# Kernel optimization log

Hardware: AMD Instinct MI355X
Metric: run time of the kernel (lower is better)

## Reference

```python
import jax, jax.numpy as jnp
import numpy as np

N_NODES = 100000
N_EDGES = 3200000
IN_DIM = 11
HID = 32


def setup_inputs() -> dict:
    key = jax.random.key(0)
    ks = jax.random.split(key, 12)
    inp = {
        "x": jax.random.normal(ks[0], (N_NODES, IN_DIM), dtype=jnp.float32),
        "edge_index": jax.random.randint(ks[1], (2, N_EDGES), 0, N_NODES, dtype=jnp.int32),
        "batch": jnp.zeros((N_NODES,), dtype=jnp.int32),
        # GCNConv layer 1 (11 -> 32)
        "W1": jax.random.normal(ks[2], (IN_DIM, HID), dtype=jnp.float32) / np.sqrt(IN_DIM),
        "b1": jnp.zeros((HID,), dtype=jnp.float32),
        # GCNConv layer 2 (32 -> 32)
        "W2": jax.random.normal(ks[3], (HID, HID), dtype=jnp.float32) / np.sqrt(HID),
        "b2": jnp.zeros((HID,), dtype=jnp.float32),
        # output MLP: 32 -> 16 -> 1
        "Wo1": jax.random.normal(ks[4], (HID, HID // 2), dtype=jnp.float32) / np.sqrt(HID),
        "bo1": jnp.zeros((HID // 2,), dtype=jnp.float32),
        "Wo2": jax.random.normal(ks[5], (HID // 2, 1), dtype=jnp.float32) / np.sqrt(HID // 2),
        "bo2": jnp.zeros((1,), dtype=jnp.float32),
    }
    return inp


def _gcn_norm(edge_index, n_nodes):
    # Add self-loops and compute symmetric normalization (PyG GCNConv default).
    loops = jnp.arange(n_nodes, dtype=edge_index.dtype)
    src = jnp.concatenate([edge_index[0], loops])
    dst = jnp.concatenate([edge_index[1], loops])
    ones = jnp.ones_like(dst, dtype=jnp.float32)
    deg = jax.ops.segment_sum(ones, dst, num_segments=n_nodes)  # degree of A+I on target side
    dinv = jax.lax.rsqrt(deg)  # deg >= 1 thanks to self-loops
    norm = dinv[src] * dinv[dst]  # [E+N]
    return src, dst, norm


def _gcn_conv(x, W, b, src, dst, norm, n_nodes):
    xw = x @ W                                   # transform first (small dim)
    msg = norm[:, None] * xw[src]                # gather + scale  [E+N, H]
    agg = jax.ops.segment_sum(msg, dst, num_segments=n_nodes)  # scatter-add
    return agg + b


def reference(x, edge_index, batch, W1, b1, W2, b2, Wo1, bo1, Wo2, bo2):
    n = x.shape[0]
    src, dst, norm = _gcn_norm(edge_index, n)
    h = jax.nn.relu(_gcn_conv(x, W1, b1, src, dst, norm, n))
    # F.dropout(training=self.training) is identity in eval mode
    h = jax.nn.relu(_gcn_conv(h, W2, b2, src, dst, norm, n))
    h = jax.nn.elu(h @ Wo1 + bo1)
    out = h @ Wo2 + bo2
    return out.squeeze(-1)  # [N]
```

## Files before the change

### kernel.cpp

```cpp
#include <hip/hip_runtime.h>
#include <hip/hip_fp16.h>
#include <math.h>

#define N_NODES 100000
#define N_EDGES 3200000
#define IN_DIM 11
#define HID 32
#define HID2 16
#define SCHUNK 100352
#define BINSHIFT 8
#define BINSZ 256
#define NB 391
#define CHUNK 8192

__global__ __launch_bounds__(1024) void k_hist(const int* __restrict__ ei,
                                               int* __restrict__ bincnt) {
    __shared__ int h[NB];
    for (int i = threadIdx.x; i < NB; i += 1024) h[i] = 0;
    __syncthreads();
    int b0 = blockIdx.x * CHUNK;
    int e1 = b0 + CHUNK; if (e1 > N_EDGES) e1 = N_EDGES;
    for (int e = b0 + threadIdx.x; e < e1; e += 1024)
        atomicAdd(&h[ei[N_EDGES + e] >> BINSHIFT], 1);
    __syncthreads();
    for (int i = threadIdx.x; i < NB; i += 1024)
        if (h[i]) atomicAdd(&bincnt[i], h[i]);
}

__global__ __launch_bounds__(1024) void k_binscatter(const int* __restrict__ ei,
                                                     const int* __restrict__ bincnt,
                                                     int* __restrict__ bincur,
                                                     unsigned* __restrict__ binbuf) {
    __shared__ int pre[NB];
    __shared__ int h[NB];
    __shared__ int base[NB];
    __shared__ int tmp[512];
    int tid = threadIdx.x;
    int v = (tid < NB) ? bincnt[tid] : 0;
    if (tid < 512) tmp[tid] = v;
    __syncthreads();
    for (int off = 1; off < 512; off <<= 1) {
        int t = (tid < 512 && tid >= off) ? tmp[tid - off] : 0;
        __syncthreads();
        if (tid < 512) tmp[tid] += t;
        __syncthreads();
    }
    if (tid < NB) pre[tid] = tmp[tid] - v;
    for (int i = tid; i < NB; i += 1024) h[i] = 0;
    __syncthreads();
    int b0 = blockIdx.x * CHUNK;
    int e1 = b0 + CHUNK; if (e1 > N_EDGES) e1 = N_EDGES;
    for (int e = b0 + tid; e < e1; e += 1024)
        atomicAdd(&h[ei[N_EDGES + e] >> BINSHIFT], 1);
    __syncthreads();
    for (int i = tid; i < NB; i += 1024) {
        int c = h[i];
        if (c) base[i] = pre[i] + atomicAdd(&bincur[i], c);
        h[i] = 0;
    }
    __syncthreads();
    for (int e = b0 + tid; e < e1; e += 1024) {
        int d = ei[N_EDGES + e];
        int s = ei[e];
        int b = d >> BINSHIFT;
        int p = base[b] + atomicAdd(&h[b], 1);
        binbuf[p] = (unsigned)s | ((unsigned)(d & (BINSZ - 1)) << 17);
    }
}

__global__ __launch_bounds__(1024) void k_binfill(const unsigned* __restrict__ binbuf,
                                                  const int* __restrict__ bincnt,
                                                  int* __restrict__ rowstart,
                                                  float* __restrict__ dinv,
                                                  int* __restrict__ csr_src) {
    int b = blockIdx.x;
    int tid = threadIdx.x;
    __shared__ int tmp[512];
    __shared__ int cnt[BINSZ];
    __shared__ int rloc[BINSZ];
    __shared__ int cur[BINSZ];
    int v = (tid < 512 && tid < b) ? bincnt[tid] : 0;
    if (tid < 512) tmp[tid] = v;
    __syncthreads();
    for (int off = 256; off >= 1; off >>= 1) {
        if (tid < off) tmp[tid] += tmp[tid + off];
        __syncthreads();
    }
    int ebeg = tmp[0];
    int eend = ebeg + bincnt[b];
    __syncthreads();
    if (tid < BINSZ) cnt[tid] = 0;
    __syncthreads();
    for (int e = ebeg + tid; e < eend; e += 1024)
        atomicAdd(&cnt[binbuf[e] >> 17], 1);
    __syncthreads();
    int c = (tid < BINSZ) ? cnt[tid] : 0;
    if (tid < BINSZ) tmp[tid] = c;
    __syncthreads();
    for (int off = 1; off < BINSZ; off <<= 1) {
        int t = (tid < BINSZ && tid >= off) ? tmp[tid - off] : 0;
        __syncthreads();
        if (tid < BINSZ) tmp[tid] += t;
        __syncthreads();
    }
    if (tid < BINSZ) {
        rloc[tid] = tmp[tid] - c;
        cur[tid] = 0;
        int node = b * BINSZ + tid;
        if (node < N_NODES) {
            rowstart[node] = ebeg + rloc[tid];
            dinv[node] = rsqrtf((float)c + 1.0f);
        }
    }
    if (b == 0 && tid == 0) rowstart[N_NODES] = N_EDGES;
    __syncthreads();
    for (int e = ebeg + tid; e < eend; e += 1024) {
        unsigned vv = binbuf[e];
        int dl = vv >> 17;
        int s = (int)(vv & 0x1FFFFu);
        int p = ebeg + rloc[dl] + atomicAdd(&cur[dl], 1);
        csr_src[p] = s;
    }
}

__global__ void k_xw1(const float* __restrict__ x, const float* __restrict__ W1,
                      const float* __restrict__ dinv, __half* __restrict__ xwh) {
    int t = blockIdx.x * blockDim.x + threadIdx.x;
    int node = t >> 5;
    int j = t & 31;
    __shared__ float sW[IN_DIM * HID];
    __shared__ float sx[8 * IN_DIM];
    for (int i = threadIdx.x; i < IN_DIM * HID; i += 256) sW[i] = W1[i];
    int base = blockIdx.x * 8;
    if (threadIdx.x < 8 * IN_DIM) sx[threadIdx.x] = x[base * IN_DIM + threadIdx.x];
    __syncthreads();
    int ln = node - base;
    float acc = 0.0f;
#pragma unroll
    for (int k = 0; k < IN_DIM; ++k)
        acc += sx[ln * IN_DIM + k] * sW[k * HID + j];
    xwh[t] = __float2half(dinv[node] * acc);
}

__device__ __forceinline__ void accum8(float* __restrict__ acc, const uint4 v) {
    float2 f0 = __half22float2(*(const __half2*)&v.x);
    float2 f1 = __half22float2(*(const __half2*)&v.y);
    float2 f2 = __half22float2(*(const __half2*)&v.z);
    float2 f3 = __half22float2(*(const __half2*)&v.w);
    acc[0] += f0.x; acc[1] += f0.y;
    acc[2] += f1.x; acc[3] += f1.y;
    acc[4] += f2.x; acc[5] += f2.y;
    acc[6] += f3.x; acc[7] += f3.y;
}

__device__ __forceinline__ void edge_accum8(int beg, int end, int q, int oj,
                                            const int* __restrict__ csr_src,
                                            const __half* __restrict__ xwh,
                                            float* __restrict__ acc) {
#pragma unroll
    for (int k = 0; k < 8; ++k) acc[k] = 0.0f;
    int e = beg;
    for (; e + 32 <= end; e += 32) {
        int s0 = csr_src[e + q];
        int s1 = csr_src[e + 8 + q];
        int s2 = csr_src[e + 16 + q];
        int s3 = csr_src[e + 24 + q];
        uint4 v0 = *(const uint4*)(xwh + ((s0 << 5) | oj));
        uint4 v1 = *(const uint4*)(xwh + ((s1 << 5) | oj));
        uint4 v2 = *(const uint4*)(xwh + ((s2 << 5) | oj));
        uint4 v3 = *(const uint4*)(xwh + ((s3 << 5) | oj));
        accum8(acc, v0); accum8(acc, v1); accum8(acc, v2); accum8(acc, v3);
    }
    if (e + 16 <= end) {
        int s0 = csr_src[e + q];
        int s1 = csr_src[e + 8 + q];
        uint4 v0 = *(const uint4*)(xwh + ((s0 << 5) | oj));
        uint4 v1 = *(const uint4*)(xwh + ((s1 << 5) | oj));
        accum8(acc, v0); accum8(acc, v1);
        e += 16;
    }
    if (e + 8 <= end) {
        int s0 = csr_src[e + q];
        uint4 v0 = *(const uint4*)(xwh + ((s0 << 5) | oj));
        accum8(acc, v0);
        e += 8;
    }
    if (e + q < end) {
        int s0 = csr_src[e + q];
        uint4 v0 = *(const uint4*)(xwh + ((s0 << 5) | oj));
        accum8(acc, v0);
    }
#pragma unroll
    for (int m = 4; m <= 16; m <<= 1) {
#pragma unroll
        for (int k = 0; k < 8; ++k) acc[k] += __shfl_xor(acc[k], m);
    }
}

__global__ __launch_bounds__(256) void k_gather_xw2(const int* __restrict__ rowstart,
                                                    const float* __restrict__ dinv,
                                                    const int* __restrict__ csr_src,
                                                    const __half* __restrict__ xwh1,
                                                    const float* __restrict__ b1,
                                                    const float* __restrict__ W2,
                                                    __half* __restrict__ xwh2) {
    __shared__ float sW2[HID * HID];
    __shared__ float sA[8][33];
    __shared__ float sH[8][33];
    for (int i = threadIdx.x; i < HID * HID; i += 256) sW2[i] = W2[i];

    int ln = threadIdx.x >> 5;
    int node = blockIdx.x * 8 + ln;
    int l = threadIdx.x & 31;
    int q = l >> 2;
    int oj = (l & 3) << 3;

    float acc[8];
    edge_accum8(rowstart[node], rowstart[node + 1], q, oj, csr_src, xwh1, acc);
    if (q == 0) {
#pragma unroll
        for (int k = 0; k < 8; ++k) sA[ln][oj + k] = acc[k];
    }
    __syncthreads();

    int j = l;
    float dd = dinv[node];
    float hv = dd * (sA[ln][j] + __half2float(xwh1[node * HID + j])) + b1[j];
    sH[ln][j] = hv > 0.0f ? hv : 0.0f;
    __syncthreads();

    float a2 = 0.0f;
#pragma unroll
    for (int k = 0; k < HID; ++k) a2 += sH[ln][k] * sW2[k * HID + j];
    xwh2[node * HID + j] = __float2half(dd * a2);
}

__global__ __launch_bounds__(256) void k_gather_mlp(const int* __restrict__ rowstart,
                                                    const float* __restrict__ dinv,
                                                    const int* __restrict__ csr_src,
                                                    const __half* __restrict__ xwh,
                                                    const float* __restrict__ b2,
                                                    const float* __restrict__ Wo1,
                                                    const float* __restrict__ bo1,
                                                    const float* __restrict__ Wo2,
                                                    const float* __restrict__ bo2,
                                                    float* __restrict__ out) {
    __shared__ float sW1[HID * HID2];
    __shared__ float sb1[HID2];
    __shared__ float sW2v[HID2];
    __shared__ float sb2[HID];
    __shared__ float sA[8][33];
    __shared__ float sH[8][33];
    for (int i = threadIdx.x; i < HID * HID2; i += 256) sW1[i] = Wo1[i];
    if (threadIdx.x < HID2) {
        sb1[threadIdx.x] = bo1[threadIdx.x];
        sW2v[threadIdx.x] = Wo2[threadIdx.x];
    }
    if (threadIdx.x < HID) sb2[threadIdx.x] = b2[threadIdx.x];

    int ln = threadIdx.x >> 5;
    int node = blockIdx.x * 8 + ln;
    int l = threadIdx.x & 31;
    int q = l >> 2;
    int oj = (l & 3) << 3;

    float acc[8];
    edge_accum8(rowstart[node], rowstart[node + 1], q, oj, csr_src, xwh, acc);
    if (q == 0) {
#pragma unroll
        for (int k = 0; k < 8; ++k) sA[ln][oj + k] = acc[k];
    }
    __syncthreads();

    int j = l;
    float dd = dinv[node];
    float hv = dd * (sA[ln][j] + __half2float(xwh[node * HID + j])) + sb2[j];
    sH[ln][j] = hv > 0.0f ? hv : 0.0f;
    __syncthreads();

    float val = 0.0f;
    if (j < HID2) {
        float a = sb1[j];
#pragma unroll
        for (int k = 0; k < HID; ++k) a += sH[ln][k] * sW1[k * HID2 + j];
        a = a > 0.0f ? a : (expf(a) - 1.0f);
        val = a * sW2v[j];
    }
#pragma unroll
    for (int d = 16; d >= 1; d >>= 1) val += __shfl_down(val, d, 32);
    if (j == 0) out[node] = val + bo2[0];
}

extern "C" void kernel_launch(void* const* d_in, const int* in_sizes, int n_in,
                              void* d_out, int out_size, void* d_ws, size_t ws_size,
                              hipStream_t stream) {
    const float* x   = (const float*)d_in[0];
    const int*   ei  = (const int*)d_in[1];
    const float* W1  = (const float*)d_in[3];
    const float* b1  = (const float*)d_in[4];
    const float* W2  = (const float*)d_in[5];
    const float* b2  = (const float*)d_in[6];
    const float* Wo1 = (const float*)d_in[7];
    const float* bo1 = (const float*)d_in[8];
    const float* Wo2 = (const float*)d_in[9];
    const float* bo2 = (const float*)d_in[10];
    float* out = (float*)d_out;

    int*      bincnt   = (int*)d_ws;
    int*      bincur   = bincnt + 512;
    int*      rowstart = bincur + 512;
    float*    dinv     = (float*)(rowstart + SCHUNK);
    int*      csr_src  = (int*)(dinv + SCHUNK);
    unsigned* binbuf   = (unsigned*)(csr_src + N_EDGES);
    __half*   XWH1     = (__half*)(binbuf + N_EDGES);
    __half*   XWH2     = XWH1 + (size_t)N_NODES * HID;

    const int BT = 256;
    int gNH  = (N_NODES * HID + BT - 1) / BT;
    int gC   = (N_EDGES + CHUNK - 1) / CHUNK;
    int gG   = N_NODES / 8;

    hipMemsetAsync(bincnt, 0, 1024 * sizeof(int), stream);
    k_hist      <<<gC, 1024, 0, stream>>>(ei, bincnt);
    k_binscatter<<<gC, 1024, 0, stream>>>(ei, bincnt, bincur, binbuf);
    k_binfill   <<<NB, 1024, 0, stream>>>(binbuf, bincnt, rowstart, dinv, csr_src);

    k_xw1<<<gNH, BT, 0, stream>>>(x, W1, dinv, XWH1);
    k_gather_xw2<<<gG, BT, 0, stream>>>(rowstart, dinv, csr_src, XWH1, b1, W2, XWH2);

    k_gather_mlp<<<gG, BT, 0, stream>>>(rowstart, dinv, csr_src, XWH2,
                                        b2, Wo1, bo1, Wo2, bo2, out);
}
```

Before: 260.1 us.

## Build CSR via global atomic degree count, scan, and atomic scatter

Replaces the two-level binned CSR construction (shared-memory histograms, bin scatter, per-bin fill) with a direct approach: global atomic degree counting, a three-kernel prefix scan, then a global atomic-cursor scatter of source indices. This drops the intermediate binbuf pass and its extra reads and writes. In exchange it relies on many global atomics on random node addresses, and the order of sources within each row becomes nondeterministic, which changes float summation order in the later gathers.

```diff
diff --git a/kernel.cpp b/kernel.cpp
--- a/kernel.cpp
+++ b/kernel.cpp
@@ -8,119 +8,84 @@
 #define HID 32
 #define HID2 16
 #define SCHUNK 100352
-#define BINSHIFT 8
-#define BINSZ 256
-#define NB 391
-#define CHUNK 8192
-
-__global__ __launch_bounds__(1024) void k_hist(const int* __restrict__ ei,
-                                               int* __restrict__ bincnt) {
-    __shared__ int h[NB];
-    for (int i = threadIdx.x; i < NB; i += 1024) h[i] = 0;
-    __syncthreads();
-    int b0 = blockIdx.x * CHUNK;
-    int e1 = b0 + CHUNK; if (e1 > N_EDGES) e1 = N_EDGES;
-    for (int e = b0 + threadIdx.x; e < e1; e += 1024)
-        atomicAdd(&h[ei[N_EDGES + e] >> BINSHIFT], 1);
-    __syncthreads();
-    for (int i = threadIdx.x; i < NB; i += 1024)
-        if (h[i]) atomicAdd(&bincnt[i], h[i]);
-}
-
-__global__ __launch_bounds__(1024) void k_binscatter(const int* __restrict__ ei,
-                                                     const int* __restrict__ bincnt,
-                                                     int* __restrict__ bincur,
-                                                     unsigned* __restrict__ binbuf) {
-    __shared__ int pre[NB];
-    __shared__ int h[NB];
-    __shared__ int base[NB];
+#define NBLK 391
+#define EB4 3125
+
+__global__ __launch_bounds__(256) void k_deg(const int* __restrict__ ei,
+                                             int* __restrict__ deg) {
+    int base = blockIdx.x * 1024 + threadIdx.x * 4;
+    int4 d4 = *(const int4*)(ei + N_EDGES + base);
+    atomicAdd(&deg[d4.x], 1);
+    atomicAdd(&deg[d4.y], 1);
+    atomicAdd(&deg[d4.z], 1);
+    atomicAdd(&deg[d4.w], 1);
+}
+
+__global__ __launch_bounds__(256) void k_scan1(const int* __restrict__ deg,
+                                               int* __restrict__ rowstart,
+                                               float* __restrict__ dinv,
+                                               int* __restrict__ blocksum) {
+    __shared__ int tmp[256];
+    int t = threadIdx.x;
+    int node = blockIdx.x * 256 + t;
+    int d = (node < N_NODES) ? deg[node] : 0;
+    tmp[t] = d;
+    __syncthreads();
+    for (int off = 1; off < 256; off <<= 1) {
+        int v = (t >= off) ? tmp[t - off] : 0;
+        __syncthreads();
+        tmp[t] += v;
+        __syncthreads();
+    }
+    if (node < N_NODES) {
+        rowstart[node] = tmp[t] - d;
+        dinv[node] = rsqrtf((float)d + 1.0f);
+    }
+    if (t == 255) blocksum[blockIdx.x] = tmp[255];
+}
+
+__global__ __launch_bounds__(512) void k_scan2(const int* __restrict__ blocksum,
+                                               int* __restrict__ basearr) {
     __shared__ int tmp[512];
-    int tid = threadIdx.x;
-    int v = (tid < NB) ? bincnt[tid] : 0;
-    if (tid < 512) tmp[tid] = v;
+    int t = threadIdx.x;
+    int v = (t < NBLK) ? blocksum[t] : 0;
+    tmp[t] = v;
     __syncthreads();
     for (int off = 1; off < 512; off <<= 1) {
-        int t = (tid < 512 && tid >= off) ? tmp[tid - off] : 0;
-        __syncthreads();
-        if (tid < 512) tmp[tid] += t;
-        __syncthreads();
-    }
-    if (tid < NB) pre[tid] = tmp[tid] - v;
-    for (int i = tid; i < NB; i += 1024) h[i] = 0;
-    __syncthreads();
-    int b0 = blockIdx.x * CHUNK;
-    int e1 = b0 + CHUNK; if (e1 > N_EDGES) e1 = N_EDGES;
-    for (int e = b0 + tid; e < e1; e += 1024)
-        atomicAdd(&h[ei[N_EDGES + e] >> BINSHIFT], 1);
-    __syncthreads();
-    for (int i = tid; i < NB; i += 1024) {
-        int c = h[i];
-        if (c) base[i] = pre[i] + atomicAdd(&bincur[i], c);
-        h[i] = 0;
-    }
-    __syncthreads();
-    for (int e = b0 + tid; e < e1; e += 1024) {
-        int d = ei[N_EDGES + e];
-        int s = ei[e];
-        int b = d >> BINSHIFT;
-        int p = base[b] + atomicAdd(&h[b], 1);
-        binbuf[p] = (unsigned)s | ((unsigned)(d & (BINSZ - 1)) << 17);
-    }
-}
-
-__global__ __launch_bounds__(1024) void k_binfill(const unsigned* __restrict__ binbuf,
-                                                  const int* __restrict__ bincnt,
-                                                  int* __restrict__ rowstart,
-                                                  float* __restrict__ dinv,
-                                                  int* __restrict__ csr_src) {
-    int b = blockIdx.x;
-    int tid = threadIdx.x;
-    __shared__ int tmp[512];
-    __shared__ int cnt[BINSZ];
-    __shared__ int rloc[BINSZ];
-    __shared__ int cur[BINSZ];
-    int v = (tid < 512 && tid < b) ? bincnt[tid] : 0;
-    if (tid < 512) tmp[tid] = v;
-    __syncthreads();
-    for (int off = 256; off >= 1; off >>= 1) {
-        if (tid < off) tmp[tid] += tmp[tid + off];
-        __syncthreads();
-    }
-    int ebeg = tmp[0];
-    int eend = ebeg + bincnt[b];
-    __syncthreads();
-    if (tid < BINSZ) cnt[tid] = 0;
-    __syncthreads();
-    for (int e = ebeg + tid; e < eend; e += 1024)
-        atomicAdd(&cnt[binbuf[e] >> 17], 1);
-    __syncthreads();
-    int c = (tid < BINSZ) ? cnt[tid] : 0;
-    if (tid < BINSZ) tmp[tid] = c;
-    __syncthreads();
-    for (int off = 1; off < BINSZ; off <<= 1) {
-        int t = (tid < BINSZ && tid >= off) ? tmp[tid - off] : 0;
-        __syncthreads();
-        if (tid < BINSZ) tmp[tid] += t;
-        __syncthreads();
-    }
-    if (tid < BINSZ) {
-        rloc[tid] = tmp[tid] - c;
-        cur[tid] = 0;
-        int node = b * BINSZ + tid;
-        if (node < N_NODES) {
-            rowstart[node] = ebeg + rloc[tid];
-            dinv[node] = rsqrtf((float)c + 1.0f);
-        }
-    }
-    if (b == 0 && tid == 0) rowstart[N_NODES] = N_EDGES;
-    __syncthreads();
-    for (int e = ebeg + tid; e < eend; e += 1024) {
-        unsigned vv = binbuf[e];
-        int dl = vv >> 17;
-        int s = (int)(vv & 0x1FFFFu);
-        int p = ebeg + rloc[dl] + atomicAdd(&cur[dl], 1);
-        csr_src[p] = s;
-    }
+        int u = (t >= off) ? tmp[t - off] : 0;
+        __syncthreads();
+        tmp[t] += u;
+        __syncthreads();
+    }
+    if (t < NBLK) basearr[t] = tmp[t] - v;
+}
+
+__global__ __launch_bounds__(256) void k_scan3(int* __restrict__ rowstart,
+                                               const int* __restrict__ basearr,
+                                               int* __restrict__ cur) {
+    int node = blockIdx.x * 256 + threadIdx.x;
+    if (node < N_NODES) {
+        int rs = rowstart[node] + basearr[blockIdx.x];
+        rowstart[node] = rs;
+        cur[node] = rs;
+    }
+    if (blockIdx.x == 0 && threadIdx.x == 0) rowstart[N_NODES] = N_EDGES;
+}
+
+__global__ __launch_bounds__(256) void k_scatter(const int* __restrict__ ei,
+                                                 int* __restrict__ cur,
+                                                 int* __restrict__ csr_src) {
+    int base = blockIdx.x * 1024 + threadIdx.x * 4;
+    int4 s4 = *(const int4*)(ei + base);
+    int4 d4 = *(const int4*)(ei + N_EDGES + base);
+    int p0 = atomicAdd(&cur[d4.x], 1);
+    int p1 = atomicAdd(&cur[d4.y], 1);
+    int p2 = atomicAdd(&cur[d4.z], 1);
+    int p3 = atomicAdd(&cur[d4.w], 1);
+    csr_src[p0] = s4.x;
+    csr_src[p1] = s4.y;
+    csr_src[p2] = s4.z;
+    csr_src[p3] = s4.w;
 }
 
 __global__ void k_xw1(const float* __restrict__ x, const float* __restrict__ W1,
@@ -306,24 +271,25 @@
     const float* bo2 = (const float*)d_in[10];
     float* out = (float*)d_out;
 
-    int*      bincnt   = (int*)d_ws;
-    int*      bincur   = bincnt + 512;
-    int*      rowstart = bincur + 512;
+    int*      blocksum = (int*)d_ws;
+    int*      basearr  = blocksum + 512;
+    int*      rowstart = basearr + 512;
     float*    dinv     = (float*)(rowstart + SCHUNK);
-    int*      csr_src  = (int*)(dinv + SCHUNK);
-    unsigned* binbuf   = (unsigned*)(csr_src + N_EDGES);
-    __half*   XWH1     = (__half*)(binbuf + N_EDGES);
+    int*      cur      = (int*)(dinv + SCHUNK);
+    int*      csr_src  = cur + SCHUNK;
+    __half*   XWH1     = (__half*)(csr_src + N_EDGES);
     __half*   XWH2     = XWH1 + (size_t)N_NODES * HID;
 
     const int BT = 256;
     int gNH  = (N_NODES * HID + BT - 1) / BT;
-    int gC   = (N_EDGES + CHUNK - 1) / CHUNK;
     int gG   = N_NODES / 8;
 
-    hipMemsetAsync(bincnt, 0, 1024 * sizeof(int), stream);
-    k_hist      <<<gC, 1024, 0, stream>>>(ei, bincnt);
-    k_binscatter<<<gC, 1024, 0, stream>>>(ei, bincnt, bincur, binbuf);
-    k_binfill   <<<NB, 1024, 0, stream>>>(binbuf, bincnt, rowstart, dinv, csr_src);
+    hipMemsetAsync(cur, 0, SCHUNK * sizeof(int), stream);
+    k_deg    <<<EB4, BT, 0, stream>>>(ei, cur);
+    k_scan1  <<<NBLK, BT, 0, stream>>>(cur, rowstart, dinv, blocksum);
+    k_scan2  <<<1, 512, 0, stream>>>(blocksum, basearr);
+    k_scan3  <<<NBLK, BT, 0, stream>>>(rowstart, basearr, cur);
+    k_scatter<<<EB4, BT, 0, stream>>>(ei, cur, csr_src);
 
     k_xw1<<<gNH, BT, 0, stream>>>(x, W1, dinv, XWH1);
     k_gather_xw2<<<gG, BT, 0, stream>>>(rowstart, dinv, csr_src, XWH1, b1, W2, XWH2);
```

After: 623.4 us. 140% more time.

## Replace atomic bin offsets with per-block count matrix and column scans

Applied to the files above, without the earlier changes.

The binning sort now writes a per-chunk, per-bin count matrix instead of using global atomics. Two small scan kernels turn that matrix into exact write offsets, so the scatter kernel no longer re-histograms its chunk. Chunks are halved and blocks shrunk to 256 threads, and binfill reads bin bounds directly instead of reducing counts per block. This trades one edge pass and the global atomics for two extra small launches, and it reuses the csr_src buffer for the count matrix.

```diff
diff --git a/kernel.cpp b/kernel.cpp
--- a/kernel.cpp
+++ b/kernel.cpp
@@ -11,55 +11,87 @@
 #define BINSHIFT 8
 #define BINSZ 256
 #define NB 391
-#define CHUNK 8192
-
-__global__ __launch_bounds__(1024) void k_hist(const int* __restrict__ ei,
-                                               int* __restrict__ bincnt) {
+#define CHUNK 4096
+#define NBC 782
+
+__global__ __launch_bounds__(256) void k_hist(const int* __restrict__ ei,
+                                              int* __restrict__ cnthist) {
     __shared__ int h[NB];
-    for (int i = threadIdx.x; i < NB; i += 1024) h[i] = 0;
+    int t = threadIdx.x;
+    for (int i = t; i < NB; i += 256) h[i] = 0;
     __syncthreads();
     int b0 = blockIdx.x * CHUNK;
     int e1 = b0 + CHUNK; if (e1 > N_EDGES) e1 = N_EDGES;
-    for (int e = b0 + threadIdx.x; e < e1; e += 1024)
+    for (int e = b0 + t; e < e1; e += 256)
         atomicAdd(&h[ei[N_EDGES + e] >> BINSHIFT], 1);
     __syncthreads();
-    for (int i = threadIdx.x; i < NB; i += 1024)
-        if (h[i]) atomicAdd(&bincnt[i], h[i]);
-}
-
-__global__ __launch_bounds__(1024) void k_binscatter(const int* __restrict__ ei,
-                                                     const int* __restrict__ bincnt,
-                                                     int* __restrict__ bincur,
-                                                     unsigned* __restrict__ binbuf) {
-    __shared__ int pre[NB];
+    for (int i = t; i < NB; i += 256)
+        cnthist[i * NBC + blockIdx.x] = h[i];
+}
+
+__global__ __launch_bounds__(256) void k_colscan(int* __restrict__ cnthist,
+                                                 int* __restrict__ colsum) {
+    __shared__ int tmp[256];
+    int i = blockIdx.x;
+    int t = threadIdx.x;
+    int v[4];
+    int s4 = 0;
+#pragma unroll
+    for (int u = 0; u < 4; ++u) {
+        int idx = t * 4 + u;
+        v[u] = (idx < NBC) ? cnthist[i * NBC + idx] : 0;
+        s4 += v[u];
+    }
+    tmp[t] = s4;
+    __syncthreads();
+    for (int off = 1; off < 256; off <<= 1) {
+        int u = (t >= off) ? tmp[t - off] : 0;
+        __syncthreads();
+        tmp[t] += u;
+        __syncthreads();
+    }
+    int base = tmp[t] - s4;
+#pragma unroll
+    for (int u = 0; u < 4; ++u) {
+        int idx = t * 4 + u;
+        if (idx < NBC) cnthist[i * NBC + idx] = base;
+        base += v[u];
+    }
+    if (t == 255) colsum[i] = tmp[255];
+}
+
+__global__ __launch_bounds__(512) void k_scanbins(const int* __restrict__ colsum,
+                                                  int* __restrict__ binbase) {
+    __shared__ int tmp[512];
+    int t = threadIdx.x;
+    int v = (t < NB) ? colsum[t] : 0;
+    tmp[t] = v;
+    __syncthreads();
+    for (int off = 1; off < 512; off <<= 1) {
+        int u = (t >= off) ? tmp[t - off] : 0;
+        __syncthreads();
+        tmp[t] += u;
+        __syncthreads();
+    }
+    if (t < NB) binbase[t] = tmp[t] - v;
+    if (t == 0) binbase[NB] = N_EDGES;
+}
+
+__global__ __launch_bounds__(256) void k_binscatter(const int* __restrict__ ei,
+                                                    const int* __restrict__ binbase,
+                                                    const int* __restrict__ cnthist,
+                                                    unsigned* __restrict__ binbuf) {
     __shared__ int h[NB];
     __shared__ int base[NB];
-    __shared__ int tmp[512];
-    int tid = threadIdx.x;
-    int v = (tid < NB) ? bincnt[tid] : 0;
-    if (tid < 512) tmp[tid] = v;
-    __syncthreads();
-    for (int off = 1; off < 512; off <<= 1) {
-        int t = (tid < 512 && tid >= off) ? tmp[tid - off] : 0;
-        __syncthreads();
-        if (tid < 512) tmp[tid] += t;
-        __syncthreads();
-    }
-    if (tid < NB) pre[tid] = tmp[tid] - v;
-    for (int i = tid; i < NB; i += 1024) h[i] = 0;
+    int t = threadIdx.x;
+    for (int i = t; i < NB; i += 256) {
+        base[i] = binbase[i] + cnthist[i * NBC + blockIdx.x];
+        h[i] = 0;
+    }
     __syncthreads();
     int b0 = blockIdx.x * CHUNK;
     int e1 = b0 + CHUNK; if (e1 > N_EDGES) e1 = N_EDGES;
-    for (int e = b0 + tid; e < e1; e += 1024)
-        atomicAdd(&h[ei[N_EDGES + e] >> BINSHIFT], 1);
-    __syncthreads();
-    for (int i = tid; i < NB; i += 1024) {
-        int c = h[i];
-        if (c) base[i] = pre[i] + atomicAdd(&bincur[i], c);
-        h[i] = 0;
-    }
-    __syncthreads();
-    for (int e = b0 + tid; e < e1; e += 1024) {
+    for (int e = b0 + t; e < e1; e += 256) {
         int d = ei[N_EDGES + e];
         int s = ei[e];
         int b = d >> BINSHIFT;
@@ -68,53 +100,40 @@
     }
 }
 
-__global__ __launch_bounds__(1024) void k_binfill(const unsigned* __restrict__ binbuf,
-                                                  const int* __restrict__ bincnt,
-                                                  int* __restrict__ rowstart,
-                                                  float* __restrict__ dinv,
-                                                  int* __restrict__ csr_src) {
-    int b = blockIdx.x;
-    int tid = threadIdx.x;
-    __shared__ int tmp[512];
-    __shared__ int cnt[BINSZ];
-    __shared__ int rloc[BINSZ];
-    __shared__ int cur[BINSZ];
-    int v = (tid < 512 && tid < b) ? bincnt[tid] : 0;
-    if (tid < 512) tmp[tid] = v;
-    __syncthreads();
-    for (int off = 256; off >= 1; off >>= 1) {
-        if (tid < off) tmp[tid] += tmp[tid + off];
-        __syncthreads();
-    }
-    int ebeg = tmp[0];
-    int eend = ebeg + bincnt[b];
-    __syncthreads();
-    if (tid < BINSZ) cnt[tid] = 0;
-    __syncthreads();
-    for (int e = ebeg + tid; e < eend; e += 1024)
+__global__ __launch_bounds__(512) void k_binfill(const unsigned* __restrict__ binbuf,
+                                                 const int* __restrict__ binbase,
+                                                 int* __restrict__ rowstart,
+                                                 float* __restrict__ dinv,
+                                                 int* __restrict__ csr_src) {
+    int b = blockIdx.x, t = threadIdx.x;
+    __shared__ int cnt[BINSZ], rloc[BINSZ], cur[BINSZ], tmp[BINSZ];
+    int ebeg = binbase[b], eend = binbase[b + 1];
+    if (t < BINSZ) cnt[t] = 0;
+    __syncthreads();
+    for (int e = ebeg + t; e < eend; e += 512)
         atomicAdd(&cnt[binbuf[e] >> 17], 1);
     __syncthreads();
-    int c = (tid < BINSZ) ? cnt[tid] : 0;
-    if (tid < BINSZ) tmp[tid] = c;
+    int c = 0;
+    if (t < BINSZ) { c = cnt[t]; tmp[t] = c; }
     __syncthreads();
     for (int off = 1; off < BINSZ; off <<= 1) {
-        int t = (tid < BINSZ && tid >= off) ? tmp[tid - off] : 0;
-        __syncthreads();
-        if (tid < BINSZ) tmp[tid] += t;
-        __syncthreads();
-    }
-    if (tid < BINSZ) {
-        rloc[tid] = tmp[tid] - c;
-        cur[tid] = 0;
-        int node = b * BINSZ + tid;
+        int u = (t < BINSZ && t >= off) ? tmp[t - off] : 0;
+        __syncthreads();
+        if (t < BINSZ) tmp[t] += u;
+        __syncthreads();
+    }
+    if (t < BINSZ) {
+        rloc[t] = tmp[t] - c;
+        cur[t] = 0;
+        int node = b * BINSZ + t;
         if (node < N_NODES) {
-            rowstart[node] = ebeg + rloc[tid];
+            rowstart[node] = ebeg + rloc[t];
             dinv[node] = rsqrtf((float)c + 1.0f);
         }
     }
-    if (b == 0 && tid == 0) rowstart[N_NODES] = N_EDGES;
-    __syncthreads();
-    for (int e = ebeg + tid; e < eend; e += 1024) {
+    if (b == 0 && t == 0) rowstart[N_NODES] = N_EDGES;
+    __syncthreads();
+    for (int e = ebeg + t; e < eend; e += 512) {
         unsigned vv = binbuf[e];
         int dl = vv >> 17;
         int s = (int)(vv & 0x1FFFFu);
@@ -306,24 +325,25 @@
     const float* bo2 = (const float*)d_in[10];
     float* out = (float*)d_out;
 
-    int*      bincnt   = (int*)d_ws;
-    int*      bincur   = bincnt + 512;
-    int*      rowstart = bincur + 512;
+    int*      colsum   = (int*)d_ws;
+    int*      binbase  = colsum + 512;
+    int*      rowstart = binbase + 512;
     float*    dinv     = (float*)(rowstart + SCHUNK);
     int*      csr_src  = (int*)(dinv + SCHUNK);
     unsigned* binbuf   = (unsigned*)(csr_src + N_EDGES);
     __half*   XWH1     = (__half*)(binbuf + N_EDGES);
     __half*   XWH2     = XWH1 + (size_t)N_NODES * HID;
+    int*      cnthist  = csr_src;
 
     const int BT = 256;
     int gNH  = (N_NODES * HID + BT - 1) / BT;
-    int gC   = (N_EDGES + CHUNK - 1) / CHUNK;
     int gG   = N_NODES / 8;
 
-    hipMemsetAsync(bincnt, 0, 1024 * sizeof(int), stream);
-    k_hist      <<<gC, 1024, 0, stream>>>(ei, bincnt);
-    k_binscatter<<<gC, 1024, 0, stream>>>(ei, bincnt, bincur, binbuf);
-    k_binfill   <<<NB, 1024, 0, stream>>>(binbuf, bincnt, rowstart, dinv, csr_src);
+    k_hist      <<<NBC, BT, 0, stream>>>(ei, cnthist);
+    k_colscan   <<<NB, BT, 0, stream>>>(cnthist, colsum);
+    k_scanbins  <<<1, 512, 0, stream>>>(colsum, binbase);
+    k_binscatter<<<NBC, BT, 0, stream>>>(ei, binbase, cnthist, binbuf);
+    k_binfill   <<<NB, 512, 0, stream>>>(binbuf, binbase, rowstart, dinv, csr_src);
 
     k_xw1<<<gNH, BT, 0, stream>>>(x, W1, dinv, XWH1);
     k_gather_xw2<<<gG, BT, 0, stream>>>(rowstart, dinv, csr_src, XWH1, b1, W2, XWH2);
```

Result: slower. 267.0 us (+2.7%).
